# Performance work log

Hardware: AMD Instinct MI355X
Metric: run time of the kernel (lower is better)

The kernel has to match this reference:

```python
import jax, jax.numpy as jnp
import numpy as np
import math

B, N, D = 2, 2048, 512   # batch, seq, input_dim
H = 8                     # num_head
DK, DV = 512, 512         # dim_k, dim_v (dim_v == input_dim for the final reshape)


def setup_inputs() -> dict:
    key = jax.random.key(0)
    ks = jax.random.split(key, 7)
    s = 1.0 / math.sqrt(D)
    return {
        "x":  jax.random.normal(ks[0], (B, N, D), jnp.float32),
        "Wq": jax.random.normal(ks[1], (H, DK, D), jnp.float32) * s,
        "bq": jax.random.normal(ks[2], (H, DK), jnp.float32) * s,
        "Wk": jax.random.normal(ks[3], (DK, D), jnp.float32) * s,
        "bk": jax.random.normal(ks[4], (DK,), jnp.float32) * s,
        "Wv": jax.random.normal(ks[5], (DV, D), jnp.float32) * s,
        "bv": jax.random.normal(ks[6], (DV,), jnp.float32) * s,
    }


def reference(x, Wq, bq, Wk, bk, Wv, bv):
    # Per-head Q projections (each head projects to full dim_k), batched as one einsum.
    Q = jnp.einsum("bnd,hkd->bhnk", x, Wq) + bq[None, :, None, :]   # [B,H,N,DK]
    K = x @ Wk.T + bk                                               # [B,N,DK] (shared)
    V = x @ Wv.T + bv                                               # [B,N,DV] (shared)
    scores = jnp.einsum("bhnk,bmk->bhnm", Q, K) / math.sqrt(DK)     # [B,H,N,N]
    A = jax.nn.softmax(scores, axis=-1)                             # softmax over keys
    At = jnp.swapaxes(A, -2, -1)                                    # quirk: transpose before V matmul
    out = jnp.einsum("bhnm,bnv->bhmv", A, V)                        # == At @ V (V broadcast over heads)
    out = out.reshape(-1, N, D)                                     # [B*H, N, D] since DV == D
    return (At, out)
```

## Files before the change

kernel.cpp:

```cpp
#include <hip/hip_runtime.h>
#include <stdint.h>

typedef __attribute__((ext_vector_type(8))) short short8;
typedef __attribute__((ext_vector_type(4))) float f4;
typedef unsigned short u16;

#define Nn 2048
#define Dd 512
#define Hh 8
#define BNrows 4096
#define SCALE 0.044194173824159216f

__device__ __forceinline__ u16 f2b(float f) {
  union { float f; uint32_t u; } c; c.f = f;
  uint32_t u = c.u;
  u += 0x7fffu + ((u >> 16) & 1u);
  return (u16)(u >> 16);
}

__device__ __forceinline__ void gload_lds16(const void* g, void* l) {
  __builtin_amdgcn_global_load_lds((const __attribute__((address_space(1))) void*)g,
                                   (__attribute__((address_space(3))) void*)l, 16, 0, 0);
}

__global__ void cvt_kernel(const float* __restrict__ src, u16* __restrict__ dst, int n8) {
  int i = blockIdx.x * 256 + threadIdx.x;
  if (i >= n8) return;
  const f4* s4 = (const f4*)src;
  f4 a = s4[2*i], b = s4[2*i+1];
  short8 o;
  o[0]=(short)f2b(a[0]); o[1]=(short)f2b(a[1]); o[2]=(short)f2b(a[2]); o[3]=(short)f2b(a[3]);
  o[4]=(short)f2b(b[0]); o[5]=(short)f2b(b[1]); o[6]=(short)f2b(b[2]); o[7]=(short)f2b(b[3]);
  ((short8*)dst)[i] = o;
}

__global__ void zero_kernel(float* __restrict__ p, int n) {
  int i = blockIdx.x * 256 + threadIdx.x;
  if (i < n) p[i] = 0.0f;
}

__global__ void recip_kernel(const float* __restrict__ s, float* __restrict__ rs, int n) {
  int i = blockIdx.x * 256 + threadIdx.x;
  if (i < n) rs[i] = 1.0f / s[i];
}

__launch_bounds__(256)
__global__ void proj_gemm(const u16* __restrict__ A, int lda,
                          const u16* __restrict__ Bm, int ldb,
                          const float* __restrict__ bias, int bias_row,
                          u16* __restrict__ C, int ldc) {
  __shared__ __align__(16) u16 Al[128*64];
  __shared__ __align__(16) u16 Bl[128*64];
  const int t = threadIdx.x, w = t >> 6, l = t & 63;
  const int m0 = blockIdx.y * 128, n0 = blockIdx.x * 128;
  const int wm = (w >> 1) * 64, wn = (w & 1) * 64;
  const int srow = l >> 3, scol = (l & 7) * 8;
  f4 acc[4][4] = {};
  for (int k0 = 0; k0 < 512; k0 += 64) {
    #pragma unroll
    for (int j = 0; j < 4; ++j) {
      const int chunk = (w << 2) + j;
      const int row = (chunk << 3) + srow;
      gload_lds16(A  + (size_t)(m0 + row) * lda + (k0 + scol), &Al[chunk << 9]);
      gload_lds16(Bm + (size_t)(n0 + row) * ldb + (k0 + scol), &Bl[chunk << 9]);
    }
    __syncthreads();
    #pragma unroll
    for (int ks = 0; ks < 64; ks += 32) {
      short8 af[4], bfr[4];
      #pragma unroll
      for (int i = 0; i < 4; ++i)
        af[i] = *(const short8*)&Al[(wm + i*16 + (l & 15)) * 64 + ks + ((l >> 4) << 3)];
      #pragma unroll
      for (int j = 0; j < 4; ++j)
        bfr[j] = *(const short8*)&Bl[(wn + j*16 + (l & 15)) * 64 + ks + ((l >> 4) << 3)];
      #pragma unroll
      for (int i = 0; i < 4; ++i)
        #pragma unroll
        for (int j = 0; j < 4; ++j)
          acc[i][j] = __builtin_amdgcn_mfma_f32_16x16x32_bf16(af[i], bfr[j], acc[i][j], 0, 0, 0);
    }
    __syncthreads();
  }
  const int cr = (l >> 4) << 2, cc = l & 15;
  #pragma unroll
  for (int i = 0; i < 4; ++i) {
    #pragma unroll
    for (int j = 0; j < 4; ++j) {
      const int col = n0 + wn + j*16 + cc;
      #pragma unroll
      for (int r = 0; r < 4; ++r) {
        const int row = m0 + wm + i*16 + cr + r;
        const float bb = bias_row ? bias[row] : bias[col];
        C[(size_t)row * ldc + col] = f2b(acc[i][j][r] + bb);
      }
    }
  }
}

__launch_bounds__(256)
__global__ void score_gemm(const u16* __restrict__ Kb, const u16* __restrict__ Qb,
                           float* __restrict__ E) {
  __shared__ __align__(16) u16 Al[128*64];
  __shared__ __align__(16) u16 Bl[128*64];
  const int t = threadIdx.x, w = t >> 6, l = t & 63;
  const int bh = blockIdx.z, b = bh >> 3, h = bh & 7;
  const u16* A  = Kb + (size_t)b * Nn * Dd;
  const u16* Bm = Qb + (size_t)b * Nn * BNrows + h * Dd;
  float* C = E + (size_t)bh * Nn * Nn;
  const int m0 = blockIdx.y * 128, n0 = blockIdx.x * 128;
  const int wm = (w >> 1) * 64, wn = (w & 1) * 64;
  const int srow = l >> 3, scol = (l & 7) * 8;
  f4 acc[4][4] = {};
  for (int k0 = 0; k0 < 512; k0 += 64) {
    #pragma unroll
    for (int j = 0; j < 4; ++j) {
      const int chunk = (w << 2) + j;
      const int row = (chunk << 3) + srow;
      gload_lds16(A  + (size_t)(m0 + row) * Dd      + (k0 + scol), &Al[chunk << 9]);
      gload_lds16(Bm + (size_t)(n0 + row) * BNrows  + (k0 + scol), &Bl[chunk << 9]);
    }
    __syncthreads();
    #pragma unroll
    for (int ks = 0; ks < 64; ks += 32) {
      short8 af[4], bfr[4];
      #pragma unroll
      for (int i = 0; i < 4; ++i)
        af[i] = *(const short8*)&Al[(wm + i*16 + (l & 15)) * 64 + ks + ((l >> 4) << 3)];
      #pragma unroll
      for (int j = 0; j < 4; ++j)
        bfr[j] = *(const short8*)&Bl[(wn + j*16 + (l & 15)) * 64 + ks + ((l >> 4) << 3)];
      #pragma unroll
      for (int i = 0; i < 4; ++i)
        #pragma unroll
        for (int j = 0; j < 4; ++j)
          acc[i][j] = __builtin_amdgcn_mfma_f32_16x16x32_bf16(af[i], bfr[j], acc[i][j], 0, 0, 0);
    }
    __syncthreads();
  }
  const int cr = (l >> 4) << 2, cc = l & 15;
  #pragma unroll
  for (int i = 0; i < 4; ++i) {
    #pragma unroll
    for (int j = 0; j < 4; ++j) {
      const int col = n0 + wn + j*16 + cc;
      #pragma unroll
      for (int r = 0; r < 4; ++r) {
        const int row = m0 + wm + i*16 + cr + r;
        C[(size_t)row * Nn + col] = __expf(acc[i][j][r] * SCALE);
      }
    }
  }
}

__global__ void colsum_kernel(const float* __restrict__ E, float* __restrict__ s) {
  const int n = blockIdx.x * 256 + threadIdx.x;
  const int mc = blockIdx.y, bh = blockIdx.z;
  const float* p = E + (size_t)bh * Nn * Nn + (size_t)mc * 256 * Nn + n;
  float a0=0,a1=0,a2=0,a3=0,a4=0,a5=0,a6=0,a7=0;
  for (int m = 0; m < 256; m += 8) {
    a0 += p[(size_t)(m+0)*Nn]; a1 += p[(size_t)(m+1)*Nn];
    a2 += p[(size_t)(m+2)*Nn]; a3 += p[(size_t)(m+3)*Nn];
    a4 += p[(size_t)(m+4)*Nn]; a5 += p[(size_t)(m+5)*Nn];
    a6 += p[(size_t)(m+6)*Nn]; a7 += p[(size_t)(m+7)*Nn];
  }
  atomicAdd(&s[bh * Nn + n], ((a0+a1)+(a2+a3)) + ((a4+a5)+(a6+a7)));
}

__launch_bounds__(256)
__global__ void out_gemm(float* __restrict__ E, const u16* __restrict__ Vt,
                         const float* __restrict__ rs, float* __restrict__ O) {
  __shared__ __align__(16) u16 Al[64*32];
  __shared__ __align__(16) u16 Bl[512*32];
  const int t = threadIdx.x, w = t >> 6, l = t & 63;
  const int mb = blockIdx.x, bh = blockIdx.y, b = bh >> 3;
  float* Ep = E + (size_t)bh * Nn * Nn + (size_t)mb * 64 * Nn;
  const float* rsp = rs + bh * Nn;
  const u16* Vp = Vt + (size_t)b * Nn;
  const int wv = w << 7;
  const int am = t >> 2, an8 = (t & 3) << 3;
  const int bvr = l >> 2, bcol = (l & 3) << 3;
  f4 acc[4][8] = {};
  for (int k0 = 0; k0 < Nn; k0 += 32) {
    #pragma unroll
    for (int j = 0; j < 8; ++j) {
      const int chunk = (w << 3) + j;
      const int vrow = (chunk << 4) + bvr;
      gload_lds16(Vp + (size_t)vrow * BNrows + k0 + bcol, &Bl[chunk << 9]);
    }
    float* ap = Ep + (size_t)am * Nn + k0 + an8;
    f4 x0 = *(const f4*)ap;
    f4 x1 = *(const f4*)(ap + 4);
    const f4 r0 = *(const f4*)(rsp + k0 + an8);
    const f4 r1 = *(const f4*)(rsp + k0 + an8 + 4);
    x0 *= r0; x1 *= r1;
    *(f4*)ap = x0; *(f4*)(ap + 4) = x1;
    short8 ab;
    ab[0]=(short)f2b(x0[0]); ab[1]=(short)f2b(x0[1]); ab[2]=(short)f2b(x0[2]); ab[3]=(short)f2b(x0[3]);
    ab[4]=(short)f2b(x1[0]); ab[5]=(short)f2b(x1[1]); ab[6]=(short)f2b(x1[2]); ab[7]=(short)f2b(x1[3]);
    *(short8*)&Al[am * 32 + an8] = ab;
    __syncthreads();
    short8 af[4];
    #pragma unroll
    for (int i = 0; i < 4; ++i)
      af[i] = *(const short8*)&Al[(i*16 + (l & 15)) * 32 + ((l >> 4) << 3)];
    #pragma unroll
    for (int j = 0; j < 8; ++j) {
      const short8 bfj = *(const short8*)&Bl[(wv + j*16 + (l & 15)) * 32 + ((l >> 4) << 3)];
      #pragma unroll
      for (int i = 0; i < 4; ++i)
        acc[i][j] = __builtin_amdgcn_mfma_f32_16x16x32_bf16(af[i], bfj, acc[i][j], 0, 0, 0);
    }
    __syncthreads();
  }
  float* Op = O + (size_t)bh * Nn * Dd + (size_t)mb * 64 * Dd;
  #pragma unroll
  for (int i = 0; i < 4; ++i)
    #pragma unroll
    for (int j = 0; j < 8; ++j)
      #pragma unroll
      for (int r = 0; r < 4; ++r)
        Op[(size_t)(i*16 + ((l >> 4) << 2) + r) * Dd + (wv + j*16 + (l & 15))] = acc[i][j][r];
}

extern "C" void kernel_launch(void* const* d_in, const int* in_sizes, int n_in,
                              void* d_out, int out_size, void* d_ws, size_t ws_size,
                              hipStream_t stream) {
  const float* x  = (const float*)d_in[0];
  const float* Wq = (const float*)d_in[1];
  const float* bq = (const float*)d_in[2];
  const float* Wk = (const float*)d_in[3];
  const float* bk = (const float*)d_in[4];
  const float* Wv = (const float*)d_in[5];
  const float* bv = (const float*)d_in[6];

  u16* xb  = (u16*)d_ws;
  u16* Wqb = xb  + (size_t)4096 * 512;
  u16* Wkb = Wqb + (size_t)4096 * 512;
  u16* Wvb = Wkb + (size_t)512 * 512;
  u16* Qb  = Wvb + (size_t)512 * 512;
  u16* Kb  = Qb  + (size_t)4096 * 4096;
  u16* Vtb = Kb  + (size_t)4096 * 512;
  float* ssum = (float*)(Vtb + (size_t)4096 * 512);
  float* rs   = ssum + 16 * 2048;

  float* Eo = (float*)d_out;
  float* Oo = Eo + (size_t)16 * 2048 * 2048;

  cvt_kernel<<<1024, 256, 0, stream>>>(x,  xb,  262144);
  cvt_kernel<<<1024, 256, 0, stream>>>(Wq, Wqb, 262144);
  cvt_kernel<<<128,  256, 0, stream>>>(Wk, Wkb, 32768);
  cvt_kernel<<<128,  256, 0, stream>>>(Wv, Wvb, 32768);
  zero_kernel<<<128, 256, 0, stream>>>(ssum, 32768);

  proj_gemm<<<dim3(32, 32), 256, 0, stream>>>(xb, 512, Wqb, 512, bq, 0, Qb, 4096);
  proj_gemm<<<dim3(4, 32),  256, 0, stream>>>(xb, 512, Wkb, 512, bk, 0, Kb, 512);
  proj_gemm<<<dim3(32, 4),  256, 0, stream>>>(Wvb, 512, xb, 512, bv, 1, Vtb, 4096);

  score_gemm<<<dim3(16, 16, 16), 256, 0, stream>>>(Kb, Qb, Eo);
  colsum_kernel<<<dim3(8, 8, 16), 256, 0, stream>>>(Eo, ssum);
  recip_kernel<<<128, 256, 0, stream>>>(ssum, rs, 32768);
  out_gemm<<<dim3(32, 16), 256, 0, stream>>>(Eo, Vtb, rs, Oo);
}
```

Before: 772.1 us.

## Fuse column-sum into score GEMM epilogue and merge prep/projection launches

Column sums of the exponentiated scores are now accumulated in the score GEMM epilogue with warp shuffles and atomics, so the separate colsum pass that re-read the whole 256 MB score tensor is gone. The four conversion kernels and the zeroing kernel become one prep launch, and the three projection GEMMs become one launch that dispatches on block index. This trades extra atomics and epilogue work in the score kernel for removing a large memory pass and several launches.

```diff
diff --git a/kernel.cpp b/kernel.cpp
--- a/kernel.cpp
+++ b/kernel.cpp
@@ -23,9 +23,21 @@
                                    (__attribute__((address_space(3))) void*)l, 16, 0, 0);
 }
 
-__global__ void cvt_kernel(const float* __restrict__ src, u16* __restrict__ dst, int n8) {
-  int i = blockIdx.x * 256 + threadIdx.x;
-  if (i >= n8) return;
+__global__ void prep_kernel(const float* __restrict__ x,  u16* __restrict__ xb,
+                            const float* __restrict__ Wq, u16* __restrict__ Wqb,
+                            const float* __restrict__ Wk, u16* __restrict__ Wkb,
+                            const float* __restrict__ Wv, u16* __restrict__ Wvb,
+                            float* __restrict__ ssum) {
+  const int g = blockIdx.x * 256 + threadIdx.x;
+  if (g >= 589824) {
+    ssum[g - 589824] = 0.0f;
+    return;
+  }
+  const float* src; u16* dst; int i;
+  if (g < 262144)      { src = x;  dst = xb;  i = g; }
+  else if (g < 524288) { src = Wq; dst = Wqb; i = g - 262144; }
+  else if (g < 557056) { src = Wk; dst = Wkb; i = g - 524288; }
+  else                 { src = Wv; dst = Wvb; i = g - 557056; }
   const f4* s4 = (const f4*)src;
   f4 a = s4[2*i], b = s4[2*i+1];
   short8 o;
@@ -34,25 +46,36 @@
   ((short8*)dst)[i] = o;
 }
 
-__global__ void zero_kernel(float* __restrict__ p, int n) {
-  int i = blockIdx.x * 256 + threadIdx.x;
-  if (i < n) p[i] = 0.0f;
-}
-
 __global__ void recip_kernel(const float* __restrict__ s, float* __restrict__ rs, int n) {
   int i = blockIdx.x * 256 + threadIdx.x;
   if (i < n) rs[i] = 1.0f / s[i];
 }
 
 __launch_bounds__(256)
-__global__ void proj_gemm(const u16* __restrict__ A, int lda,
-                          const u16* __restrict__ Bm, int ldb,
-                          const float* __restrict__ bias, int bias_row,
-                          u16* __restrict__ C, int ldc) {
+__global__ void proj_all(const u16* __restrict__ xb, const u16* __restrict__ Wqb,
+                         const u16* __restrict__ Wkb, const u16* __restrict__ Wvb,
+                         const float* __restrict__ bq, const float* __restrict__ bk,
+                         const float* __restrict__ bv,
+                         u16* __restrict__ Qb, u16* __restrict__ Kb, u16* __restrict__ Vtb) {
   __shared__ __align__(16) u16 Al[128*64];
   __shared__ __align__(16) u16 Bl[128*64];
+  const int bid = blockIdx.x;
+  const u16 *A, *Bm; u16* C;
+  const float* bias;
+  int lda, ldb, ldc, bias_row, m0, n0;
+  if (bid < 1024) {
+    A = xb; lda = 512; Bm = Wqb; ldb = 512; bias = bq; bias_row = 0;
+    C = Qb; ldc = 4096; n0 = (bid & 31) * 128; m0 = (bid >> 5) * 128;
+  } else if (bid < 1152) {
+    const int id = bid - 1024;
+    A = xb; lda = 512; Bm = Wkb; ldb = 512; bias = bk; bias_row = 0;
+    C = Kb; ldc = 512; n0 = (id & 3) * 128; m0 = (id >> 2) * 128;
+  } else {
+    const int id = bid - 1152;
+    A = Wvb; lda = 512; Bm = xb; ldb = 512; bias = bv; bias_row = 1;
+    C = Vtb; ldc = 4096; n0 = (id & 31) * 128; m0 = (id >> 5) * 128;
+  }
   const int t = threadIdx.x, w = t >> 6, l = t & 63;
-  const int m0 = blockIdx.y * 128, n0 = blockIdx.x * 128;
   const int wm = (w >> 1) * 64, wn = (w & 1) * 64;
   const int srow = l >> 3, scol = (l & 7) * 8;
   f4 acc[4][4] = {};
@@ -100,7 +123,7 @@
 
 __launch_bounds__(256)
 __global__ void score_gemm(const u16* __restrict__ Kb, const u16* __restrict__ Qb,
-                           float* __restrict__ E) {
+                           float* __restrict__ E, float* __restrict__ ssum) {
   __shared__ __align__(16) u16 Al[128*64];
   __shared__ __align__(16) u16 Bl[128*64];
   const int t = threadIdx.x, w = t >> 6, l = t & 63;
@@ -139,6 +162,7 @@
     __syncthreads();
   }
   const int cr = (l >> 4) << 2, cc = l & 15;
+  float psum[4] = {0.f, 0.f, 0.f, 0.f};
   #pragma unroll
   for (int i = 0; i < 4; ++i) {
     #pragma unroll
@@ -147,24 +171,20 @@
       #pragma unroll
       for (int r = 0; r < 4; ++r) {
         const int row = m0 + wm + i*16 + cr + r;
-        C[(size_t)row * Nn + col] = __expf(acc[i][j][r] * SCALE);
+        const float e = __expf(acc[i][j][r] * SCALE);
+        C[(size_t)row * Nn + col] = e;
+        psum[j] += e;
       }
     }
   }
-}
-
-__global__ void colsum_kernel(const float* __restrict__ E, float* __restrict__ s) {
-  const int n = blockIdx.x * 256 + threadIdx.x;
-  const int mc = blockIdx.y, bh = blockIdx.z;
-  const float* p = E + (size_t)bh * Nn * Nn + (size_t)mc * 256 * Nn + n;
-  float a0=0,a1=0,a2=0,a3=0,a4=0,a5=0,a6=0,a7=0;
-  for (int m = 0; m < 256; m += 8) {
-    a0 += p[(size_t)(m+0)*Nn]; a1 += p[(size_t)(m+1)*Nn];
-    a2 += p[(size_t)(m+2)*Nn]; a3 += p[(size_t)(m+3)*Nn];
-    a4 += p[(size_t)(m+4)*Nn]; a5 += p[(size_t)(m+5)*Nn];
-    a6 += p[(size_t)(m+6)*Nn]; a7 += p[(size_t)(m+7)*Nn];
-  }
-  atomicAdd(&s[bh * Nn + n], ((a0+a1)+(a2+a3)) + ((a4+a5)+(a6+a7)));
+  float* sp = ssum + bh * Nn + n0 + wn;
+  #pragma unroll
+  for (int j = 0; j < 4; ++j) {
+    float p = psum[j];
+    p += __shfl_xor(p, 16);
+    p += __shfl_xor(p, 32);
+    if (l < 16) atomicAdd(&sp[j*16 + l], p);
+  }
 }
 
 __launch_bounds__(256)
@@ -247,18 +267,9 @@
   float* Eo = (float*)d_out;
   float* Oo = Eo + (size_t)16 * 2048 * 2048;
 
-  cvt_kernel<<<1024, 256, 0, stream>>>(x,  xb,  262144);
-  cvt_kernel<<<1024, 256, 0, stream>>>(Wq, Wqb, 262144);
-  cvt_kernel<<<128,  256, 0, stream>>>(Wk, Wkb, 32768);
-  cvt_kernel<<<128,  256, 0, stream>>>(Wv, Wvb, 32768);
-  zero_kernel<<<128, 256, 0, stream>>>(ssum, 32768);
-
-  proj_gemm<<<dim3(32, 32), 256, 0, stream>>>(xb, 512, Wqb, 512, bq, 0, Qb, 4096);
-  proj_gemm<<<dim3(4, 32),  256, 0, stream>>>(xb, 512, Wkb, 512, bk, 0, Kb, 512);
-  proj_gemm<<<dim3(32, 4),  256, 0, stream>>>(Wvb, 512, xb, 512, bv, 1, Vtb, 4096);
-
-  score_gemm<<<dim3(16, 16, 16), 256, 0, stream>>>(Kb, Qb, Eo);
-  colsum_kernel<<<dim3(8, 8, 16), 256, 0, stream>>>(Eo, ssum);
+  prep_kernel<<<2432, 256, 0, stream>>>(x, xb, Wq, Wqb, Wk, Wkb, Wv, Wvb, ssum);
+  proj_all<<<1280, 256, 0, stream>>>(xb, Wqb, Wkb, Wvb, bq, bk, bv, Qb, Kb, Vtb);
+  score_gemm<<<dim3(16, 16, 16), 256, 0, stream>>>(Kb, Qb, Eo, ssum);
   recip_kernel<<<128, 256, 0, stream>>>(ssum, rs, 32768);
   out_gemm<<<dim3(32, 16), 256, 0, stream>>>(Eo, Vtb, rs, Oo);
 }
```

After: 687.2 us. 1.12x faster.
